# Optimization experiments

Hardware: AMD Instinct MI355X
Metric: run time of the kernel (lower is better)

Reference implementation:

```python
import jax, jax.numpy as jnp
import numpy as np

RATIO = 4   # compression ratio (group size)
H = 6       # index heads
D = 64      # index head dim = max(8, 768//6//2)
TOPK = 8    # index_topk
EPS = 1e-6  # rms_norm eps


def rms_norm(x):
    return x * jax.lax.rsqrt(jnp.mean(jnp.square(x), axis=-1, keepdims=True) + EPS)


def setup_inputs() -> dict:
    key = jax.random.key(0)
    k1, k2, k3, k4, k5 = jax.random.split(key, 5)
    B, T, E = 4, 4096, 768
    s = 0.02
    return {
        "x": jax.random.normal(k1, (B, T, E), jnp.float32),
        "wq": jax.random.normal(k2, (E, H * D), jnp.float32) * s,
        "wk": jax.random.normal(k3, (E, H * D), jnp.float32) * s,
        "wg": jax.random.normal(k4, (E, H * D), jnp.float32) * s,
        "ape": jax.random.normal(k5, (RATIO, H, D), jnp.float32) * s,
    }


def reference(x, wq, wk, wg, ape):
    B, T, E = x.shape
    G = -(-T // RATIO)          # ceil(T / ratio)
    pad = G * RATIO - T

    # --- compress keys: gated pooling over ratio-groups ---
    k = (x @ wk).reshape(B, T, H, D)
    gate = (x @ wg).reshape(B, T, H, D)
    if pad:
        k = jnp.pad(k, ((0, 0), (0, pad), (0, 0), (0, 0)))
        gate = jnp.pad(gate, ((0, 0), (0, pad), (0, 0), (0, 0)), constant_values=-jnp.inf)
    k = k.reshape(B, G, RATIO, H, D)
    gate = gate.reshape(B, G, RATIO, H, D) + ape[None, None]
    w = jax.nn.softmax(gate.astype(jnp.float32), axis=2).astype(k.dtype)
    keys = rms_norm(jnp.sum(k * w, axis=2))           # [B,G,H,D]
    group_ends = jnp.minimum(jnp.arange(RATIO - 1, G * RATIO, RATIO), T - 1)  # [G]

    # --- query-key scores ---
    q = rms_norm((x @ wq).reshape(B, T, H, D))
    scores = jnp.einsum('bthd,bghd->bhtg', q, keys) * (D ** -0.5)
    scores = jnp.mean(scores, axis=1)                 # [B,T,G]

    # --- causal mask over group ends, then top-k selection ---
    causal = group_ends[None, None, :] <= jnp.arange(T)[None, :, None]  # [1,T,G]
    scores = jnp.where(causal, scores, -jnp.inf)
    topk = min(TOPK, G)
    _, sel = jax.lax.top_k(scores, topk)              # [B,T,topk]

    # scatter selected indices into boolean mask
    bi = jnp.arange(B)[:, None, None]
    ti = jnp.arange(T)[None, :, None]
    mask = jnp.zeros((B, T, G), dtype=bool).at[bi, ti, sel].set(True)
    return (mask & causal, group_ends)
```

## Files before the change

### kernel.cpp

```cpp
#include <hip/hip_runtime.h>
#include <hip/hip_bf16.h>
#include <math.h>

#define B_    4
#define T_    4096
#define E_    768
#define H_    6
#define D_    64
#define HD_   384
#define G_    1024
#define RATIO_ 4
#define TOPK_ 8
#define MT_   (B_*T_)
#define NS_   1152

typedef __attribute__((ext_vector_type(8))) short short8;
typedef __attribute__((ext_vector_type(4))) float f32x4;
typedef __hip_bfloat16 bf16;

#define GLD16(g, l) __builtin_amdgcn_global_load_lds( \
    (const __attribute__((address_space(1))) void*)(g), \
    (__attribute__((address_space(3))) void*)(l), 16, 0, 0)

static __device__ __forceinline__ unsigned short f2bf(float f) {
  bf16 h = __float2bfloat16(f);
  return __builtin_bit_cast(unsigned short, h);
}
static __device__ __forceinline__ unsigned umax_(unsigned a, unsigned b) { return a > b ? a : b; }
static __device__ __forceinline__ unsigned umin_(unsigned a, unsigned b) { return a > b ? b : a; }

__global__ __launch_bounds__(256) void cvt_fused(
    const float* __restrict__ xin, const float* __restrict__ wq,
    const float* __restrict__ wk, const float* __restrict__ wg,
    bf16* __restrict__ xout, bf16* __restrict__ wsout)
{
  __shared__ float t[32][33];
  const int bid = blockIdx.x;
  if (bid < 6144) {
    size_t i = (size_t)bid * 256 + threadIdx.x;
    const float4* p = reinterpret_cast<const float4*>(xin) + i * 2;
    float4 v0 = p[0], v1 = p[1];
    float f[8] = {v0.x, v0.y, v0.z, v0.w, v1.x, v1.y, v1.z, v1.w};
    union { unsigned short u[8]; short8 v; } r;
#pragma unroll
    for (int k = 0; k < 8; ++k) r.u[k] = f2bf(f[k]);
    *reinterpret_cast<short8*>(xout + i * 8) = r.v;
    return;
  }
  const int wb = bid - 6144;
  const int z = wb / 288;
  const int rr = wb - z * 288;
  const int bx = rr % 24, by = rr / 24;
  const float* src = z == 0 ? wq : (z == 1 ? wk : wg);
  int r = threadIdx.x >> 5, c = threadIdx.x & 31;
  int k0 = bx * 32, n0 = by * 32;
#pragma unroll
  for (int i = 0; i < 4; ++i)
    t[r + i * 8][c] = src[(size_t)(k0 + r + i * 8) * HD_ + n0 + c];
  __syncthreads();
#pragma unroll
  for (int i = 0; i < 4; ++i) {
    int cc = n0 + r + i * 8;
    int ro = (z == 0) ? cc : 384 + ((cc >> 4) << 5) + ((z - 1) << 4) + (cc & 15);
    wsout[(size_t)ro * E_ + k0 + c] = __float2bfloat16(t[c][r + i * 8]);
  }
}

__global__ __launch_bounds__(256, 3) void gemm_qkg_mfma(
    const bf16* __restrict__ X, const bf16* __restrict__ Ws,
    const float* __restrict__ ape, bf16* __restrict__ Q,
    bf16* __restrict__ keys)
{
  __shared__ bf16 lds[2][8192];
  const int tid = threadIdx.x;
  const int lane = tid & 63, wv = tid >> 6;
  const int ll = lane & 15, lh = lane >> 4;
  const int m0 = blockIdx.x * 128, n0 = blockIdx.y * 128;
  const int srow = tid >> 3;
  const int sslot = (((tid & 7) ^ ((tid >> 3) & 7)) << 3);
  const bf16* pS = Ws + (size_t)(n0 + srow) * E_ + sslot;
  const bf16* pA0 = X + (size_t)(m0 + wv * 32 + ll) * E_ + lh * 8;
  const bf16* pA1 = pA0 + (size_t)16 * E_;

#define STAGE(b, k0) do { \
    char* base_ = (char*)&lds[b][0] + tid * 16; \
    GLD16(pS + (k0),            base_); \
    GLD16(pS + 32 * E_ + (k0),  base_ + 4096); \
    GLD16(pS + 64 * E_ + (k0),  base_ + 8192); \
    GLD16(pS + 96 * E_ + (k0),  base_ + 12288); \
  } while (0)
#define LOAD_A(dst, k0) do { \
    dst[0][0] = *reinterpret_cast<const short8*>(pA0 + (k0)); \
    dst[0][1] = *reinterpret_cast<const short8*>(pA0 + (k0) + 32); \
    dst[1][0] = *reinterpret_cast<const short8*>(pA1 + (k0)); \
    dst[1][1] = *reinterpret_cast<const short8*>(pA1 + (k0) + 32); \
  } while (0)

  f32x4 acc[2][8];
#pragma unroll
  for (int m = 0; m < 2; ++m)
#pragma unroll
    for (int n = 0; n < 8; ++n) acc[m][n] = (f32x4){0.f, 0.f, 0.f, 0.f};

  short8 curA[2][2], nxtA[2][2];
  LOAD_A(curA, 0);
  STAGE(0, 0);
#pragma unroll
  for (int m = 0; m < 2; ++m)
#pragma unroll
    for (int s = 0; s < 2; ++s) nxtA[m][s] = curA[m][s];

#pragma unroll
  for (int k = 0; k < 12; ++k) {
    const int k0 = k * 64;
    if (k < 11) {
      LOAD_A(nxtA, k0 + 64);
      STAGE((k + 1) & 1, k0 + 64);
    }
    if (k < 11) asm volatile("s_waitcnt vmcnt(8)" ::: "memory");
    else        asm volatile("s_waitcnt vmcnt(0)" ::: "memory");
    __builtin_amdgcn_s_barrier();
    __builtin_amdgcn_sched_barrier(0);
    const bf16* Lb = &lds[k & 1][0];
    short8 b0[8];
#pragma unroll
    for (int n = 0; n < 8; ++n)
      b0[n] = *reinterpret_cast<const short8*>(
          &Lb[(n * 16 + ll) * 64 + ((lh ^ (ll & 7)) << 3)]);
    asm volatile("s_waitcnt lgkmcnt(0)" ::: "memory");
    __builtin_amdgcn_sched_barrier(0);
#pragma unroll
    for (int m = 0; m < 2; ++m)
#pragma unroll
      for (int n = 0; n < 8; ++n)
        acc[m][n] = __builtin_amdgcn_mfma_f32_16x16x32_bf16(curA[m][0], b0[n], acc[m][n], 0, 0, 0);
    short8 b1[8];
#pragma unroll
    for (int n = 0; n < 8; ++n)
      b1[n] = *reinterpret_cast<const short8*>(
          &Lb[(n * 16 + ll) * 64 + (((4 + lh) ^ (ll & 7)) << 3)]);
    asm volatile("s_waitcnt lgkmcnt(0)" ::: "memory");
    __builtin_amdgcn_sched_barrier(0);
    __builtin_amdgcn_s_barrier();
#pragma unroll
    for (int m = 0; m < 2; ++m)
#pragma unroll
      for (int n = 0; n < 8; ++n)
        acc[m][n] = __builtin_amdgcn_mfma_f32_16x16x32_bf16(curA[m][1], b1[n], acc[m][n], 0, 0, 0);
#pragma unroll
    for (int m = 0; m < 2; ++m)
#pragma unroll
      for (int s = 0; s < 2; ++s) curA[m][s] = nxtA[m][s];
  }
#undef STAGE
#undef LOAD_A

  if (blockIdx.y < 3) {
#pragma unroll
    for (int m = 0; m < 2; ++m)
#pragma unroll
      for (int j = 0; j < 4; ++j) {
        int row = m0 + wv * 32 + m * 16 + lh * 4 + j;
#pragma unroll
        for (int h = 0; h < 2; ++h) {
          float ss = 0.f;
#pragma unroll
          for (int n = 4 * h; n < 4 * h + 4; ++n) ss += acc[m][n][j] * acc[m][n][j];
          ss += __shfl_xor(ss, 1, 64); ss += __shfl_xor(ss, 2, 64);
          ss += __shfl_xor(ss, 4, 64); ss += __shfl_xor(ss, 8, 64);
          float scl = rsqrtf(ss * (1.0f / D_) + 1e-6f);
#pragma unroll
          for (int n = 4 * h; n < 4 * h + 4; ++n)
            Q[(size_t)row * HD_ + n0 + n * 16 + ll] =
                __float2bfloat16(acc[m][n][j] * scl);
        }
      }
  } else {
    const int hcb = (n0 - 384) >> 1;
    float apev[4][4];
#pragma unroll
    for (int p = 0; p < 4; ++p) {
      int hc = hcb + p * 16 + ll;
#pragma unroll
      for (int j = 0; j < 4; ++j) apev[p][j] = ape[j * HD_ + hc];
    }
#pragma unroll
    for (int m = 0; m < 2; ++m) {
      float pooled[4];
#pragma unroll
      for (int p = 0; p < 4; ++p) {
        float g0 = acc[m][2 * p + 1][0] + apev[p][0];
        float g1 = acc[m][2 * p + 1][1] + apev[p][1];
        float g2 = acc[m][2 * p + 1][2] + apev[p][2];
        float g3 = acc[m][2 * p + 1][3] + apev[p][3];
        float mx = fmaxf(fmaxf(g0, g1), fmaxf(g2, g3));
        float e0 = expf(g0 - mx), e1 = expf(g1 - mx);
        float e2 = expf(g2 - mx), e3 = expf(g3 - mx);
        float inv = 1.0f / (e0 + e1 + e2 + e3);
        pooled[p] = (acc[m][2 * p][0] * e0 + acc[m][2 * p][1] * e1 +
                     acc[m][2 * p][2] * e2 + acc[m][2 * p][3] * e3) * inv;
      }
      float ss = pooled[0] * pooled[0] + pooled[1] * pooled[1] +
                 pooled[2] * pooled[2] + pooled[3] * pooled[3];
      ss += __shfl_xor(ss, 1, 64); ss += __shfl_xor(ss, 2, 64);
      ss += __shfl_xor(ss, 4, 64); ss += __shfl_xor(ss, 8, 64);
      float scl = rsqrtf(ss * (1.0f / D_) + 1e-6f);
      int prow = (m0 >> 2) + wv * 8 + m * 4 + lh;
#pragma unroll
      for (int p = 0; p < 4; ++p)
        keys[(size_t)prow * HD_ + hcb + p * 16 + ll] =
            __float2bfloat16(pooled[p] * scl);
    }
  }
}

#define CEx(a, bb) { unsigned h_ = umax_(a, bb), l_ = umin_(a, bb); a = h_; bb = l_; }
#define MERGE4() \
  _Pragma("unroll") \
  for (int st = 0; st < 2; ++st) { \
    const int off = 16 << st; \
    unsigned p0 = (unsigned)__shfl_xor((int)v0, off, 64); \
    unsigned p1 = (unsigned)__shfl_xor((int)v1, off, 64); \
    unsigned p2 = (unsigned)__shfl_xor((int)v2, off, 64); \
    unsigned p3 = (unsigned)__shfl_xor((int)v3, off, 64); \
    unsigned p4 = (unsigned)__shfl_xor((int)v4, off, 64); \
    unsigned p5 = (unsigned)__shfl_xor((int)v5, off, 64); \
    unsigned p6 = (unsigned)__shfl_xor((int)v6, off, 64); \
    unsigned p7 = (unsigned)__shfl_xor((int)v7, off, 64); \
    unsigned w0 = umax_(v0, p7), w1 = umax_(v1, p6); \
    unsigned w2 = umax_(v2, p5), w3 = umax_(v3, p4); \
    unsigned w4 = umax_(v4, p3), w5 = umax_(v5, p2); \
    unsigned w6 = umax_(v6, p1), w7 = umax_(v7, p0); \
    CEx(w0, w4); CEx(w1, w5); CEx(w2, w6); CEx(w3, w7); \
    CEx(w0, w2); CEx(w1, w3); CEx(w4, w6); CEx(w5, w7); \
    CEx(w0, w1); CEx(w2, w3); CEx(w4, w5); CEx(w6, w7); \
    v0 = w0; v1 = w1; v2 = w2; v3 = w3; v4 = w4; v5 = w5; v6 = w6; v7 = w7; \
  }

__global__ __launch_bounds__(128, 2) void score_topk8(
    const bf16* __restrict__ Qall, const bf16* __restrict__ Kall,
    int* __restrict__ mask, int* __restrict__ ends)
{
  __shared__ bf16 kbuf[2][12288];
  const int x = blockIdx.x;
  const int b = blockIdx.y;
  const int s = (b < 2) ? x : 127 - x;
  const int R0 = s << 5;
  const int tid = threadIdx.x;
  const int w = tid >> 6;
  const int lane = tid & 63;
  const int ll = lane & 15, lh = lane >> 4;

  if (x == 0 && b == 0) {
    int g = tid;
#pragma unroll
    for (int c = 0; c < 8; ++c, g += 128) {
      int e = (g << 2) + 3;
      ends[g] = e < T_ - 1 ? e : T_ - 1;
    }
  }

  int* mbase = mask + ((size_t)b * T_ + R0) * G_;
  {
    int4* m4 = reinterpret_cast<int4*>(mbase);
    const int4 z = make_int4(0, 0, 0, 0);
#pragma unroll
    for (int i = 0; i < 64; ++i) m4[i * 128 + tid] = z;
  }

  const bf16* Qb = Qall + (size_t)b * T_ * HD_;
  const bf16* Kb = Kall + (size_t)b * G_ * HD_;
  const int t = R0 + 16 * w + ll;
  const int gmax = (t + 1) >> 2;
  const int ntw = ((((R0 + 16 * w) >> 2) + 4) + 31) >> 5;
  const int nt  = ((((R0 + 16) >> 2) + 4) + 31) >> 5;

  const bf16* ksrc[12];
  int sdst[12];
#pragma unroll
  for (int i = 0; i < 12; ++i) {
    int u = (12 * w + i) * 64 + lane;
    int r = u / 48, sp = u - r * 48;
    int sl = sp ^ (r & 7);
    ksrc[i] = Kb + (size_t)r * HD_ + sl * 8;
    sdst[i] = u * 16;
  }
  short8 qf[12];
  {
    const bf16* pQ = Qb + (size_t)t * HD_ + lh * 8;
#pragma unroll
    for (int k = 0; k < 12; ++k)
      qf[k] = *reinterpret_cast<const short8*>(pQ + k * 32);
  }

#define KSTAGE(bf, g0) do { \
    char* bb_ = (char*)&kbuf[bf][0]; \
    _Pragma("unroll") \
    for (int i = 0; i < 12; ++i) \
      GLD16(ksrc[i] + (size_t)(g0) * HD_, bb_ + sdst[i]); \
  } while (0)

  unsigned v0 = 0, v1 = 0, v2 = 0, v3 = 0, v4 = 0, v5 = 0, v6 = 0, v7 = 0;
#define INS(xx) do { unsigned k_ = (xx), t_; \
    t_ = umax_(v0, k_); k_ = umin_(v0, k_); v0 = t_; \
    t_ = umax_(v1, k_); k_ = umin_(v1, k_); v1 = t_; \
    t_ = umax_(v2, k_); k_ = umin_(v2, k_); v2 = t_; \
    t_ = umax_(v3, k_); k_ = umin_(v3, k_); v3 = t_; \
    t_ = umax_(v4, k_); k_ = umin_(v4, k_); v4 = t_; \
    t_ = umax_(v5, k_); k_ = umin_(v5, k_); v5 = t_; \
    t_ = umax_(v6, k_); k_ = umin_(v6, k_); v6 = t_; \
    t_ = umax_(v7, k_); k_ = umin_(v7, k_); v7 = t_; } while (0)

  KSTAGE(0, 0);
  for (int mg = 0; mg < nt; ++mg) {
    if (mg + 1 < nt) {
      KSTAGE((mg + 1) & 1, (mg + 1) * 32);
      asm volatile("s_waitcnt vmcnt(12)" ::: "memory");
    } else {
      asm volatile("s_waitcnt vmcnt(0)" ::: "memory");
    }
    __builtin_amdgcn_s_barrier();
    __builtin_amdgcn_sched_barrier(0);
    if (mg < ntw) {
      const char* Lb = (const char*)&kbuf[mg & 1][0];
      f32x4 acc0 = (f32x4){0.f, 0.f, 0.f, 0.f};
      f32x4 acc1 = (f32x4){0.f, 0.f, 0.f, 0.f};
#pragma unroll
      for (int kk = 0; kk < 12; ++kk) {
        int sl = 4 * kk + lh;
        short8 k0 = *reinterpret_cast<const short8*>(
            Lb + (size_t)ll * 768 + ((sl ^ (ll & 7)) << 4));
        short8 k1 = *reinterpret_cast<const short8*>(
            Lb + (size_t)(16 + ll) * 768 + ((sl ^ (ll & 7)) << 4));
        acc0 = __builtin_amdgcn_mfma_f32_16x16x32_bf16(k0, qf[kk], acc0, 0, 0, 0);
        acc1 = __builtin_amdgcn_mfma_f32_16x16x32_bf16(k1, qf[kk], acc1, 0, 0, 0);
      }
      const int g0 = mg * 32;
#pragma unroll
      for (int j = 0; j < 4; ++j) {
        int g = g0 + lh * 4 + j;
        float xv = acc0[j] + 512.0f;
        unsigned key = (g < gmax)
            ? ((__builtin_bit_cast(unsigned, xv) & 0xFFFFFC00u) |
               (unsigned)(1023 - g))
            : 0u;
        INS(key);
      }
#pragma unroll
      for (int j = 0; j < 4; ++j) {
        int g = g0 + 16 + lh * 4 + j;
        float xv = acc1[j] + 512.0f;
        unsigned key = (g < gmax)
            ? ((__builtin_bit_cast(unsigned, xv) & 0xFFFFFC00u) |
               (unsigned)(1023 - g))
            : 0u;
        INS(key);
      }
    }
    __builtin_amdgcn_s_barrier();
  }
#undef INS
#undef KSTAGE

  MERGE4();

  __syncthreads();
  if (lh == 0) {
    int* rb = mbase + (size_t)(16 * w + ll) * G_;
    if (v0) rb[1023 - (v0 & 1023)] = 1;
    if (v1) rb[1023 - (v1 & 1023)] = 1;
    if (v2) rb[1023 - (v2 & 1023)] = 1;
    if (v3) rb[1023 - (v3 & 1023)] = 1;
    if (v4) rb[1023 - (v4 & 1023)] = 1;
    if (v5) rb[1023 - (v5 & 1023)] = 1;
    if (v6) rb[1023 - (v6 & 1023)] = 1;
    if (v7) rb[1023 - (v7 & 1023)] = 1;
  }
}

extern "C" void kernel_launch(void* const* d_in, const int* in_sizes, int n_in,
                              void* d_out, int out_size, void* d_ws, size_t ws_size,
                              hipStream_t stream)
{
  const float* x   = (const float*)d_in[0];
  const float* wq  = (const float*)d_in[1];
  const float* wk  = (const float*)d_in[2];
  const float* wg  = (const float*)d_in[3];
  const float* ape = (const float*)d_in[4];

  bf16* Ws   = (bf16*)d_ws;
  bf16* qb   = Ws + (size_t)NS_ * E_;
  bf16* keys = qb + (size_t)MT_ * HD_;

  bf16* xb = (bf16*)d_out;

  cvt_fused<<<dim3(6144 + 864), dim3(256), 0, stream>>>(x, wq, wk, wg, xb, Ws);

  gemm_qkg_mfma<<<dim3(MT_ / 128, NS_ / 128), dim3(256), 0, stream>>>(
      xb, Ws, ape, qb, keys);

  score_topk8<<<dim3(128, B_), dim3(128), 0, stream>>>(
      qb, keys, (int*)d_out, (int*)d_out + (size_t)B_ * T_ * G_);
}
```

Before: 103.8 us.

## Split score/top-k key tiles across wave pairs and merge partial top-8 via LDS

Doubles the score_topk8 block to 256 threads so that two waves share each 16-row query strip, with each wave handling alternate 32-group key tiles. The two partial top-8 lists are then merged through a small shared-memory buffer with a bitonic step before the mask is written. Key staging and mask zeroing are spread over the extra threads. The aim is more parallelism for the long causal rows that dominate the tail, at the cost of an extra LDS merge and lower per-wave utilization when tile counts are odd.

```diff
diff --git a/kernel.cpp b/kernel.cpp
--- a/kernel.cpp
+++ b/kernel.cpp
@@ -237,24 +237,27 @@
     v0 = w0; v1 = w1; v2 = w2; v3 = w3; v4 = w4; v5 = w5; v6 = w6; v7 = w7; \
   }
 
-__global__ __launch_bounds__(128, 2) void score_topk8(
+__global__ __launch_bounds__(256, 2) void score_topk8(
     const bf16* __restrict__ Qall, const bf16* __restrict__ Kall,
     int* __restrict__ mask, int* __restrict__ ends)
 {
   __shared__ bf16 kbuf[2][12288];
+  __shared__ unsigned top2[2][16][8];
   const int x = blockIdx.x;
   const int b = blockIdx.y;
   const int s = (b < 2) ? x : 127 - x;
   const int R0 = s << 5;
   const int tid = threadIdx.x;
   const int w = tid >> 6;
+  const int p = w >> 1;
+  const int sub = w & 1;
   const int lane = tid & 63;
   const int ll = lane & 15, lh = lane >> 4;
 
   if (x == 0 && b == 0) {
     int g = tid;
 #pragma unroll
-    for (int c = 0; c < 8; ++c, g += 128) {
+    for (int c = 0; c < 4; ++c, g += 256) {
       int e = (g << 2) + 3;
       ends[g] = e < T_ - 1 ? e : T_ - 1;
     }
@@ -265,21 +268,21 @@
     int4* m4 = reinterpret_cast<int4*>(mbase);
     const int4 z = make_int4(0, 0, 0, 0);
 #pragma unroll
-    for (int i = 0; i < 64; ++i) m4[i * 128 + tid] = z;
+    for (int i = 0; i < 32; ++i) m4[i * 256 + tid] = z;
   }
 
   const bf16* Qb = Qall + (size_t)b * T_ * HD_;
   const bf16* Kb = Kall + (size_t)b * G_ * HD_;
-  const int t = R0 + 16 * w + ll;
+  const int t = R0 + 16 * p + ll;
   const int gmax = (t + 1) >> 2;
-  const int ntw = ((((R0 + 16 * w) >> 2) + 4) + 31) >> 5;
+  const int ntw = ((((R0 + 16 * p) >> 2) + 4) + 31) >> 5;
   const int nt  = ((((R0 + 16) >> 2) + 4) + 31) >> 5;
 
-  const bf16* ksrc[12];
-  int sdst[12];
-#pragma unroll
-  for (int i = 0; i < 12; ++i) {
-    int u = (12 * w + i) * 64 + lane;
+  const bf16* ksrc[6];
+  int sdst[6];
+#pragma unroll
+  for (int i = 0; i < 6; ++i) {
+    int u = i * 256 + tid;
     int r = u / 48, sp = u - r * 48;
     int sl = sp ^ (r & 7);
     ksrc[i] = Kb + (size_t)r * HD_ + sl * 8;
@@ -296,7 +299,7 @@
 #define KSTAGE(bf, g0) do { \
     char* bb_ = (char*)&kbuf[bf][0]; \
     _Pragma("unroll") \
-    for (int i = 0; i < 12; ++i) \
+    for (int i = 0; i < 6; ++i) \
       GLD16(ksrc[i] + (size_t)(g0) * HD_, bb_ + sdst[i]); \
   } while (0)
 
@@ -315,13 +318,13 @@
   for (int mg = 0; mg < nt; ++mg) {
     if (mg + 1 < nt) {
       KSTAGE((mg + 1) & 1, (mg + 1) * 32);
-      asm volatile("s_waitcnt vmcnt(12)" ::: "memory");
+      asm volatile("s_waitcnt vmcnt(6)" ::: "memory");
     } else {
       asm volatile("s_waitcnt vmcnt(0)" ::: "memory");
     }
     __builtin_amdgcn_s_barrier();
     __builtin_amdgcn_sched_barrier(0);
-    if (mg < ntw) {
+    if (mg < ntw && (mg & 1) == sub) {
       const char* Lb = (const char*)&kbuf[mg & 1][0];
       f32x4 acc0 = (f32x4){0.f, 0.f, 0.f, 0.f};
       f32x4 acc1 = (f32x4){0.f, 0.f, 0.f, 0.f};
@@ -364,17 +367,33 @@
 
   MERGE4();
 
+  if (sub == 1 && lh == 0) {
+    unsigned* tp = &top2[p][ll][0];
+    tp[0] = v0; tp[1] = v1; tp[2] = v2; tp[3] = v3;
+    tp[4] = v4; tp[5] = v5; tp[6] = v6; tp[7] = v7;
+  }
   __syncthreads();
-  if (lh == 0) {
-    int* rb = mbase + (size_t)(16 * w + ll) * G_;
-    if (v0) rb[1023 - (v0 & 1023)] = 1;
-    if (v1) rb[1023 - (v1 & 1023)] = 1;
-    if (v2) rb[1023 - (v2 & 1023)] = 1;
-    if (v3) rb[1023 - (v3 & 1023)] = 1;
-    if (v4) rb[1023 - (v4 & 1023)] = 1;
-    if (v5) rb[1023 - (v5 & 1023)] = 1;
-    if (v6) rb[1023 - (v6 & 1023)] = 1;
-    if (v7) rb[1023 - (v7 & 1023)] = 1;
+
+  if (sub == 0 && lh == 0) {
+    const unsigned* tp = &top2[p][ll][0];
+    unsigned u0 = tp[0], u1 = tp[1], u2 = tp[2], u3 = tp[3];
+    unsigned u4 = tp[4], u5 = tp[5], u6 = tp[6], u7 = tp[7];
+    unsigned w0 = umax_(v0, u7), w1 = umax_(v1, u6);
+    unsigned w2 = umax_(v2, u5), w3 = umax_(v3, u4);
+    unsigned w4 = umax_(v4, u3), w5 = umax_(v5, u2);
+    unsigned w6 = umax_(v6, u1), w7 = umax_(v7, u0);
+    CEx(w0, w4); CEx(w1, w5); CEx(w2, w6); CEx(w3, w7);
+    CEx(w0, w2); CEx(w1, w3); CEx(w4, w6); CEx(w5, w7);
+    CEx(w0, w1); CEx(w2, w3); CEx(w4, w5); CEx(w6, w7);
+    int* rb = mbase + (size_t)(16 * p + ll) * G_;
+    if (w0) rb[1023 - (w0 & 1023)] = 1;
+    if (w1) rb[1023 - (w1 & 1023)] = 1;
+    if (w2) rb[1023 - (w2 & 1023)] = 1;
+    if (w3) rb[1023 - (w3 & 1023)] = 1;
+    if (w4) rb[1023 - (w4 & 1023)] = 1;
+    if (w5) rb[1023 - (w5 & 1023)] = 1;
+    if (w6) rb[1023 - (w6 & 1023)] = 1;
+    if (w7) rb[1023 - (w7 & 1023)] = 1;
   }
 }
 
@@ -399,6 +418,6 @@
   gemm_qkg_mfma<<<dim3(MT_ / 128, NS_ / 128), dim3(256), 0, stream>>>(
       xb, Ws, ape, qb, keys);
 
-  score_topk8<<<dim3(128, B_), dim3(128), 0, stream>>>(
+  score_topk8<<<dim3(128, B_), dim3(256), 0, stream>>>(
       qb, keys, (int*)d_out, (int*)d_out + (size_t)B_ * T_ * G_);
 }
```

After: 106.5 us. +2.6%, slower.
